# Kernel optimization log

Hardware: AMD Instinct MI355X
Metric: run time of the kernel (lower is better)

The kernel has to match this reference:

```python
import jax, jax.numpy as jnp
import numpy as np

N, E, IN, H, OUT = 100000, 1600000, 128, 128, 64


def setup_inputs() -> dict:
    key = jax.random.key(0)
    ks = jax.random.split(key, 7)
    x = jax.random.normal(ks[0], (N, IN), dtype=jnp.float32)
    edge_index = jax.random.randint(ks[1], (2, E), 0, N, dtype=jnp.int32)
    # Glorot-style scaled params (PyG SAGEConv: lin_l has bias, lin_r does not)
    s1 = 1.0 / np.sqrt(IN)
    s2 = 1.0 / np.sqrt(H)
    W1_l = jax.random.normal(ks[2], (H, IN), dtype=jnp.float32) * s1
    W1_r = jax.random.normal(ks[3], (H, IN), dtype=jnp.float32) * s1
    b1 = jnp.zeros((H,), dtype=jnp.float32)
    W2_l = jax.random.normal(ks[4], (OUT, H), dtype=jnp.float32) * s2
    W2_r = jax.random.normal(ks[5], (OUT, H), dtype=jnp.float32) * s2
    b2 = jnp.zeros((OUT,), dtype=jnp.float32)
    return {"x": x, "W1_l": W1_l, "W1_r": W1_r, "b1": b1,
            "W2_l": W2_l, "W2_r": W2_r, "b2": b2, "edge_index": edge_index}


def _sage_conv(x, edge_index, W_l, W_r, b):
    # mean-aggregate source-node features at target nodes, then linear + root term
    src, dst = edge_index[0], edge_index[1]
    n = x.shape[0]
    msgs = x[src]                                                   # [E, d]
    agg = jax.ops.segment_sum(msgs, dst, num_segments=n)            # [N, d]
    deg = jax.ops.segment_sum(jnp.ones((src.shape[0],), x.dtype), dst, num_segments=n)
    mean = agg / jnp.clip(deg, 1.0)[:, None]                        # zero-deg nodes stay 0
    return mean @ W_l.T + b + x @ W_r.T


def reference(x, W1_l, W1_r, b1, W2_l, W2_r, b2, edge_index):
    h = _sage_conv(x, edge_index, W1_l, W1_r, b1)
    h = jax.nn.relu(h)  # dropout p=0.0 -> identity
    out = _sage_conv(h, edge_index, W2_l, W2_r, b2)
    return out
```

## Files before the change

### kernel.cpp

```cpp
#include <hip/hip_runtime.h>


typedef unsigned int uint32;
typedef short bf16x4 __attribute__((ext_vector_type(4)));
typedef short bf16x8 __attribute__((ext_vector_type(8)));
typedef float f32x16 __attribute__((ext_vector_type(16)));
typedef float f32x2 __attribute__((ext_vector_type(2)));

#define PSTR 264

__device__ __forceinline__ uint32 pack_bf16_rne(float a, float b) {
    uint32 ua = __float_as_uint(a);
    uint32 ub = __float_as_uint(b);
    uint32 ra = (ua + 0x7fffu + ((ua >> 16) & 1u)) >> 16;
    uint32 rb = (ub + 0x7fffu + ((ub >> 16) & 1u)) >> 16;
    return ra | (rb << 16);
}
__device__ __forceinline__ float bf_lo(uint32 v) { return __uint_as_float(v << 16); }
__device__ __forceinline__ float bf_hi(uint32 v) { return __uint_as_float(v & 0xffff0000u); }

__device__ __forceinline__ short rne16(float v, float* back) {
    uint32 u = __float_as_uint(v);
    uint32 r = (u + 0x7fffu + ((u >> 16) & 1u)) >> 16;
    *back = __uint_as_float(r << 16);
    return (short)r;
}

__global__ void k_prep(const float* __restrict__ x, uint32* __restrict__ xb,
                       long n4,
                       const float* __restrict__ W1l, const float* __restrict__ W1r,
                       const float* __restrict__ W2l, const float* __restrict__ W2r,
                       short* __restrict__ W1pH, short* __restrict__ W1pL,
                       short* __restrict__ W2pH, short* __restrict__ W2pL) {
    long i = (long)blockIdx.x * blockDim.x + threadIdx.x;
    float back;
    if (i < n4) {
        float4 v = ((const float4*)x)[i];
        short h0 = rne16(v.x, &back);
        short h1 = rne16(v.y, &back);
        short h2 = rne16(v.z, &back);
        short h3 = rne16(v.w, &back);
        uint2 o;
        o.x = (uint32)(unsigned short)h0 | ((uint32)(unsigned short)h1 << 16);
        o.y = (uint32)(unsigned short)h2 | ((uint32)(unsigned short)h3 << 16);
        ((uint2*)xb)[i] = o;
        return;
    }
    int i2 = (int)(i - n4);
    if (i2 < 32768) {
        int j = i2 >> 8, k = i2 & 255;
        float v = (k < 128) ? W1l[j * 128 + k] : W1r[j * 128 + k - 128];
        float hb;
        short hs = rne16(v, &hb);
        short ls = rne16(v - hb, &back);
        int idx = (k >> 3) * 1024 + j * 8 + (k & 7);
        W1pH[idx] = hs;
        W1pL[idx] = ls;
    } else if (i2 < 32768 + 16384) {
        int i3 = i2 - 32768;
        int j = i3 >> 7, k = i3 & 127;
        float v = (j < 64) ? W2l[j * 128 + k] : W2r[(j - 64) * 128 + k];
        float hb;
        short hs = rne16(v, &hb);
        short ls = rne16(v - hb, &back);
        int idx = (k >> 3) * 1024 + j * 8 + (k & 7);
        W2pH[idx] = hs;
        W2pL[idx] = ls;
    }
}


__global__ void k_bcount(const int* __restrict__ ei, int E, int NB,
                         int* __restrict__ bucket_cnt) {
    __shared__ int hist[1024];
    int t = threadIdx.x;
    for (int i = t; i < NB; i += 256) hist[i] = 0;
    __syncthreads();
    int stride = gridDim.x * 256;
    for (int e = blockIdx.x * 256 + t; e < E; e += stride)
        atomicAdd(&hist[ei[E + e] >> 8], 1);
    __syncthreads();
    for (int i = t; i < NB; i += 256) {
        int c = hist[i];
        if (c) atomicAdd(&bucket_cnt[i], c);
    }
}

__global__ void k_bscan(const int* __restrict__ bucket_cnt, int NB, int E,
                        int* __restrict__ bucket_off, int* __restrict__ bucket_cur) {
    __shared__ int s[1024];
    int t = threadIdx.x;
    int v = (t < NB) ? bucket_cnt[t] : 0;
    s[t] = v;
    __syncthreads();
    for (int o = 1; o < 1024; o <<= 1) {
        int u = (t >= o) ? s[t - o] : 0;
        __syncthreads();
        s[t] += u;
        __syncthreads();
    }
    int ex = s[t] - v;
    if (t < NB) { bucket_off[t] = ex; bucket_cur[t] = ex; }
    if (t == NB - 1) bucket_off[NB] = ex + v;
}

__global__ void k_bscatter(const int* __restrict__ ei, int E, int NB,
                           int* __restrict__ bucket_cur, uint32* __restrict__ eb) {
    __shared__ int hist[1024];
    __shared__ int base[1024];
    int t = threadIdx.x;
    for (int i = t; i < NB; i += 256) hist[i] = 0;
    __syncthreads();
    int stride = gridDim.x * 256;
    for (int e = blockIdx.x * 256 + t; e < E; e += stride)
        atomicAdd(&hist[ei[E + e] >> 8], 1);
    __syncthreads();
    for (int i = t; i < NB; i += 256) {
        int c = hist[i];
        base[i] = c ? atomicAdd(&bucket_cur[i], c) : 0;
        hist[i] = 0;
    }
    __syncthreads();
    for (int e = blockIdx.x * 256 + t; e < E; e += stride) {
        int d = ei[E + e];
        int b = d >> 8;
        int r = atomicAdd(&hist[b], 1);
        eb[base[b] + r] = ((uint32)(d & 255) << 24) | (uint32)ei[e];
    }
}

__global__ void k_bfinal(const uint32* __restrict__ eb,
                         const int* __restrict__ bucket_off,
                         int* __restrict__ row_ptr, int* __restrict__ col,
                         int N, int E) {
    __shared__ int deg[256];
    __shared__ int sc[256];
    __shared__ int cur[256];
    int b = blockIdx.x;
    int t = threadIdx.x;
    int beg = bucket_off[b], end = bucket_off[b + 1];
    deg[t] = 0;
    __syncthreads();
    for (int e = beg + t; e < end; e += 256)
        atomicAdd(&deg[eb[e] >> 24], 1);
    __syncthreads();
    int v = deg[t];
    sc[t] = v;
    __syncthreads();
    for (int o = 1; o < 256; o <<= 1) {
        int u = (t >= o) ? sc[t - o] : 0;
        __syncthreads();
        sc[t] += u;
        __syncthreads();
    }
    int ex = sc[t] - v;
    int node = b * 256 + t;
    if (node < N) row_ptr[node] = beg + ex;
    if (b == gridDim.x - 1 && t == 0) row_ptr[N] = E;
    cur[t] = ex;
    __syncthreads();
    for (int e = beg + t; e < end; e += 256) {
        uint32 u = eb[e];
        int r = atomicAdd(&cur[u >> 24], 1);
        col[beg + r] = (int)(u & 0xFFFFFFu);
    }
}


__global__ __launch_bounds__(256, 4) void k_fused(
        const int* __restrict__ rp, const int* __restrict__ col,
        const uint32* __restrict__ xb,
        const short* __restrict__ W1pH, const short* __restrict__ W1pL,
        const short* __restrict__ W2pH, const short* __restrict__ W2pL,
        const float* __restrict__ b1, const float* __restrict__ b2,
        unsigned short* __restrict__ hl, float* __restrict__ hr, int N) {
    __shared__ short smH[16 * PSTR];
    __shared__ short smL[16 * PSTR];
    int t = threadIdx.x;
    int w = t >> 6, lane = t & 63;
    int g = lane >> 4, f = lane & 15;
    int node0 = blockIdx.x * 32;
    const uint4* xb4 = (const uint4*)xb;

    int base = node0 + 8 * w;
    int rpi = base + lane;
    if (rpi > N) rpi = N;
    int rpv = rp[rpi];

    for (int i = 0; i < 8; i++) {
        int lr = 8 * w + i;
        int beg = __builtin_amdgcn_readfirstlane(__shfl(rpv, i));
        int end = __builtin_amdgcn_readfirstlane(__shfl(rpv, i + 1));
        f32x2 sA[4];
#pragma unroll
        for (int j = 0; j < 4; j++) sA[j] = (f32x2){0.f, 0.f};

#define ACC_RAW(v)                                                      \
    { sA[0] += (f32x2){bf_lo(v.x), __uint_as_float(v.x)};               \
      sA[1] += (f32x2){bf_lo(v.y), __uint_as_float(v.y)};               \
      sA[2] += (f32x2){bf_lo(v.z), __uint_as_float(v.z)};               \
      sA[3] += (f32x2){bf_lo(v.w), __uint_as_float(v.w)}; }

        int e = beg;
        for (; e + 16 <= end; e += 16) {
            uint4 cv = *(const uint4*)(col + e + 4 * g);
            uint4 v0 = xb4[(size_t)cv.x * 16 + f];
            uint4 v1 = xb4[(size_t)cv.y * 16 + f];
            uint4 v2 = xb4[(size_t)cv.z * 16 + f];
            uint4 v3 = xb4[(size_t)cv.w * 16 + f];
            ACC_RAW(v0); ACC_RAW(v1); ACC_RAW(v2); ACC_RAW(v3);
        }
        for (; e + 8 <= end; e += 8) {
            uint2 cv = *(const uint2*)(col + e + 2 * g);
            uint4 v0 = xb4[(size_t)cv.x * 16 + f];
            uint4 v1 = xb4[(size_t)cv.y * 16 + f];
            ACC_RAW(v0); ACC_RAW(v1);
        }
        int rem = end - e;
        if (2 * g < rem) {
            uint4 v0 = xb4[(size_t)col[e + 2 * g] * 16 + f];
            ACC_RAW(v0);
        }
        if (2 * g + 1 < rem) {
            uint4 v0 = xb4[(size_t)col[e + 2 * g + 1] * 16 + f];
            ACC_RAW(v0);
        }
#undef ACC_RAW
#pragma unroll
        for (int p = 0; p < 4; p++) {
            sA[p].x += __shfl_xor(sA[p].x, 16);
            sA[p].y += __shfl_xor(sA[p].y, 16);
            sA[p].x += __shfl_xor(sA[p].x, 32);
            sA[p].y += __shfl_xor(sA[p].y, 32);
        }
        float inv = 1.0f / (float)max(end - beg, 1);
        float m0 = sA[g].x * inv, m1 = sA[g].y * inv;
        float b_;
        short h0 = rne16(m0, &b_);
        float bk0 = b_;
        short l0 = rne16(m0 - bk0, &b_);
        short h1 = rne16(m1, &b_);
        float bk1 = b_;
        short l1 = rne16(m1 - bk1, &b_);
        uint32 H = (uint32)(unsigned short)h0 | ((uint32)(unsigned short)h1 << 16);
        uint32 L = (uint32)(unsigned short)l0 | ((uint32)(unsigned short)l1 << 16);
        *(uint32*)&smH[f * PSTR + lr * 8 + 2 * g] = H;
        *(uint32*)&smL[f * PSTR + lr * 8 + 2 * g] = L;
    }
    __syncthreads();

    int m = lane & 31, hh = lane >> 5;
    int mynode = node0 + m;
    const short* xbs = (const short*)xb;
    f32x16 acc;
#pragma unroll
    for (int r = 0; r < 16; r++) acc[r] = 0.f;
#pragma unroll
    for (int kc = 0; kc < 8; kc++) {
        int c = 2 * kc + hh;
        bf16x8 bH = *(const bf16x8*)&smH[c * PSTR + m * 8];
        bf16x8 bL = *(const bf16x8*)&smL[c * PSTR + m * 8];
        bf16x8 xH = *(const bf16x8*)(xbs + (size_t)mynode * 128 + c * 8);
        bf16x8 aH1 = *(const bf16x8*)(W1pH + c * 1024 + (32 * w + m) * 8);
        bf16x8 aL1 = *(const bf16x8*)(W1pL + c * 1024 + (32 * w + m) * 8);
        bf16x8 aH2 = *(const bf16x8*)(W1pH + (16 + c) * 1024 + (32 * w + m) * 8);
        bf16x8 aL2 = *(const bf16x8*)(W1pL + (16 + c) * 1024 + (32 * w + m) * 8);
        acc = __builtin_amdgcn_mfma_f32_32x32x16_bf16(aH1, bH, acc, 0, 0, 0);
        acc = __builtin_amdgcn_mfma_f32_32x32x16_bf16(aL1, bH, acc, 0, 0, 0);
        acc = __builtin_amdgcn_mfma_f32_32x32x16_bf16(aH1, bL, acc, 0, 0, 0);
        acc = __builtin_amdgcn_mfma_f32_32x32x16_bf16(aH2, xH, acc, 0, 0, 0);
        acc = __builtin_amdgcn_mfma_f32_32x32x16_bf16(aL2, xH, acc, 0, 0, 0);
    }

    uint2 oh[4], ol[4];
#pragma unroll
    for (int rg = 0; rg < 4; rg++) {
        int j0 = 32 * w + 8 * rg + 4 * hh;
        float4 bv = *(const float4*)(b1 + j0);
        float bb[4] = {bv.x, bv.y, bv.z, bv.w};
        short hs[4], ls[4];
#pragma unroll
        for (int q = 0; q < 4; q++) {
            float v = fmaxf(acc[4 * rg + q] + bb[q], 0.f);
            float back;
            hs[q] = rne16(v, &back);
            ls[q] = rne16(v - back, &back);
        }
        oh[rg].x = (uint32)(unsigned short)hs[0] | ((uint32)(unsigned short)hs[1] << 16);
        oh[rg].y = (uint32)(unsigned short)hs[2] | ((uint32)(unsigned short)hs[3] << 16);
        ol[rg].x = (uint32)(unsigned short)ls[0] | ((uint32)(unsigned short)ls[1] << 16);
        ol[rg].y = (uint32)(unsigned short)ls[2] | ((uint32)(unsigned short)ls[3] << 16);
    }
    __syncthreads();
#pragma unroll
    for (int rg = 0; rg < 4; rg++) {
        int idx = (4 * w + rg) * PSTR + m * 8 + 4 * hh;
        *(uint2*)&smH[idx] = oh[rg];
        *(uint2*)&smL[idx] = ol[rg];
    }
    __syncthreads();

#pragma unroll
    for (int r = 0; r < 16; r++) acc[r] = 0.f;
#pragma unroll
    for (int kc = 0; kc < 8; kc++) {
        int c = 2 * kc + hh;
        bf16x8 bH = *(const bf16x8*)&smH[c * PSTR + m * 8];
        bf16x8 bL = *(const bf16x8*)&smL[c * PSTR + m * 8];
        bf16x8 aH = *(const bf16x8*)(W2pH + c * 1024 + (32 * w + m) * 8);
        bf16x8 aL = *(const bf16x8*)(W2pL + c * 1024 + (32 * w + m) * 8);
        acc = __builtin_amdgcn_mfma_f32_32x32x16_bf16(aH, bH, acc, 0, 0, 0);
        acc = __builtin_amdgcn_mfma_f32_32x32x16_bf16(aL, bH, acc, 0, 0, 0);
        acc = __builtin_amdgcn_mfma_f32_32x32x16_bf16(aH, bL, acc, 0, 0, 0);
    }
    if (mynode >= N) return;
    if (w < 2) {
#pragma unroll
        for (int rg = 0; rg < 4; rg++) {
            int j0 = 32 * w + 8 * rg + 4 * hh;
            uint2 o;
            o.x = pack_bf16_rne(acc[4 * rg + 0], acc[4 * rg + 1]);
            o.y = pack_bf16_rne(acc[4 * rg + 2], acc[4 * rg + 3]);
            *(uint2*)&hl[(size_t)mynode * 64 + j0] = o;
        }
    } else {
#pragma unroll
        for (int rg = 0; rg < 4; rg++) {
            int j0 = 32 * (w - 2) + 8 * rg + 4 * hh;
            float4 bv = *(const float4*)(b2 + j0);
            float4 o;
            o.x = acc[4 * rg + 0] + bv.x;
            o.y = acc[4 * rg + 1] + bv.y;
            o.z = acc[4 * rg + 2] + bv.z;
            o.w = acc[4 * rg + 3] + bv.w;
            *(float4*)&hr[(size_t)mynode * 64 + j0] = o;
        }
    }
}


__global__ void k_agg_out(const int* __restrict__ rp, const int* __restrict__ col,
                          const uint32* __restrict__ hl, const float* __restrict__ hr,
                          float* __restrict__ out, int N) {
    int node = blockIdx.x * 4 + (threadIdx.x >> 6);
    if (node >= N) return;
    node = __builtin_amdgcn_readfirstlane(node);
    int lane = threadIdx.x & 63;
    int g = lane >> 3;
    int f = lane & 7;
    int beg = rp[node], end = rp[node + 1];
    const uint4* hl4 = (const uint4*)hl;
    f32x2 sA[4];
#pragma unroll
    for (int j = 0; j < 4; j++) sA[j] = (f32x2){0.f, 0.f};

#define ACC_MSK(v)                                          \
    { sA[0] += (f32x2){bf_lo(v.x), bf_hi(v.x)};             \
      sA[1] += (f32x2){bf_lo(v.y), bf_hi(v.y)};             \
      sA[2] += (f32x2){bf_lo(v.z), bf_hi(v.z)};             \
      sA[3] += (f32x2){bf_lo(v.w), bf_hi(v.w)}; }

    int e = beg;
    for (; e + 16 <= end; e += 16) {
        uint2 cv = *(const uint2*)(col + e + 2 * g);
        uint4 v0 = hl4[(size_t)cv.x * 8 + f];
        uint4 v1 = hl4[(size_t)cv.y * 8 + f];
        ACC_MSK(v0); ACC_MSK(v1);
    }
    for (; e + 8 <= end; e += 8) {
        uint4 v0 = hl4[(size_t)col[e + g] * 8 + f];
        ACC_MSK(v0);
    }
    int rem = end - e;
    if (g < rem) {
        uint4 v0 = hl4[(size_t)col[e + g] * 8 + f];
        ACC_MSK(v0);
    }
#undef ACC_MSK
#pragma unroll
    for (int p = 0; p < 4; p++) {
        sA[p].x += __shfl_xor(sA[p].x, 8);
        sA[p].y += __shfl_xor(sA[p].y, 8);
        sA[p].x += __shfl_xor(sA[p].x, 16);
        sA[p].y += __shfl_xor(sA[p].y, 16);
        sA[p].x += __shfl_xor(sA[p].x, 32);
        sA[p].y += __shfl_xor(sA[p].y, 32);
    }
    if (g == 0) {
        float inv = 1.0f / (float)max(end - beg, 1);
        const float* hrp = hr + (size_t)node * 64 + f * 8;
        float4 h0 = *(const float4*)(hrp);
        float4 h1 = *(const float4*)(hrp + 4);
        float4 o0, o1;
        o0.x = sA[0].x * inv + h0.x;
        o0.y = sA[0].y * inv + h0.y;
        o0.z = sA[1].x * inv + h0.z;
        o0.w = sA[1].y * inv + h0.w;
        o1.x = sA[2].x * inv + h1.x;
        o1.y = sA[2].y * inv + h1.y;
        o1.z = sA[3].x * inv + h1.z;
        o1.w = sA[3].y * inv + h1.w;
        float* op = out + (size_t)node * 64 + f * 8;
        *(float4*)(op) = o0;
        *(float4*)(op + 4) = o1;
    }
}

extern "C" void kernel_launch(void* const* d_in, const int* in_sizes, int n_in,
                              void* d_out, int out_size, void* d_ws, size_t ws_size,
                              hipStream_t stream) {
    const float* x   = (const float*)d_in[0];
    const float* W1l = (const float*)d_in[1];
    const float* W1r = (const float*)d_in[2];
    const float* b1  = (const float*)d_in[3];
    const float* W2l = (const float*)d_in[4];
    const float* W2r = (const float*)d_in[5];
    const float* b2  = (const float*)d_in[6];
    const int*   ei  = (const int*)d_in[7];
    int N = in_sizes[0] / 128;
    int E = in_sizes[7] / 2;
    int NB = (N + 255) >> 8;
    int mb = (N + 31) / 32;
    int Np = ((N + 127) / 128) * 128;
    float* out = (float*)d_out;

    char* w = (char*)d_ws;
    size_t off = 0;
    auto alloc = [&](size_t bytes) -> char* {
        char* p = w + off;
        off += (bytes + 255) & ~(size_t)255;
        return p;
    };
    int*   row_ptr = (int*)alloc((size_t)(N + 1) * 4);
    int*   bcnt    = (int*)alloc((size_t)(NB + 1) * 4);
    int*   boff    = (int*)alloc((size_t)(NB + 1) * 4);
    int*   bcur    = (int*)alloc((size_t)(NB + 1) * 4);
    short* W1pH    = (short*)alloc(32768 * 2);
    short* W1pL    = (short*)alloc(32768 * 2);
    short* W2pH    = (short*)alloc(16384 * 2);
    short* W2pL    = (short*)alloc(16384 * 2);
    int*   col     = (int*)alloc((size_t)E * 4);
    uint32* xb     = (uint32*)alloc((size_t)Np * 64 * 4);
    float*  hr     = (float*)alloc((size_t)Np * 64 * 4);
    unsigned short* hl = (unsigned short*)alloc((size_t)N * 64 * 2);
    uint32* eb = (uint32*)hl;

    hipMemsetAsync(bcnt, 0, (size_t)NB * 4, stream);
    long n4 = (long)N * 32;
    long prep_items = n4 + 32768 + 16384;
    k_prep<<<(int)((prep_items + 255) / 256), 256, 0, stream>>>(
        x, xb, n4, W1l, W1r, W2l, W2r, W1pH, W1pL, W2pH, W2pL);
    k_bcount<<<256, 256, 0, stream>>>(ei, E, NB, bcnt);
    k_bscan<<<1, 1024, 0, stream>>>(bcnt, NB, E, boff, bcur);
    k_bscatter<<<128, 256, 0, stream>>>(ei, E, NB, bcur, eb);
    k_bfinal<<<NB, 256, 0, stream>>>(eb, boff, row_ptr, col, N, E);

    k_fused<<<mb, 256, 0, stream>>>(row_ptr, col, xb, W1pH, W1pL, W2pH, W2pL,
                                    b1, b2, hl, hr, N);
    int ab = (N + 3) / 4;
    k_agg_out<<<ab, 256, 0, stream>>>(row_ptr, col, (const uint32*)hl, hr, out, N);
}
```

Before: 316.8 us.

## Merge CSR-build launches and prefetch neighbor rows across nodes in aggregation

```diff
diff --git a/kernel.cpp b/kernel.cpp
--- a/kernel.cpp
+++ b/kernel.cpp
@@ -26,13 +26,31 @@
     return (short)r;
 }
 
-__global__ void k_prep(const float* __restrict__ x, uint32* __restrict__ xb,
-                       long n4,
-                       const float* __restrict__ W1l, const float* __restrict__ W1r,
-                       const float* __restrict__ W2l, const float* __restrict__ W2r,
-                       short* __restrict__ W1pH, short* __restrict__ W1pL,
-                       short* __restrict__ W2pH, short* __restrict__ W2pL) {
-    long i = (long)blockIdx.x * blockDim.x + threadIdx.x;
+__global__ void k_prepcount(const float* __restrict__ x, uint32* __restrict__ xb,
+                            long n4,
+                            const float* __restrict__ W1l, const float* __restrict__ W1r,
+                            const float* __restrict__ W2l, const float* __restrict__ W2r,
+                            short* __restrict__ W1pH, short* __restrict__ W1pL,
+                            short* __restrict__ W2pH, short* __restrict__ W2pL,
+                            const int* __restrict__ ei, int E, int NB,
+                            int* __restrict__ bucket_cnt, int prep_blocks) {
+    __shared__ int hist[512];
+    int t = threadIdx.x;
+    if ((int)blockIdx.x >= prep_blocks) {
+        int bb = (int)blockIdx.x - prep_blocks;
+        for (int i = t; i < NB; i += 256) hist[i] = 0;
+        __syncthreads();
+        int stride = 256 * 256;
+        for (int e = bb * 256 + t; e < E; e += stride)
+            atomicAdd(&hist[ei[E + e] >> 8], 1);
+        __syncthreads();
+        for (int i = t; i < NB; i += 256) {
+            int c = hist[i];
+            if (c) atomicAdd(&bucket_cnt[i], c);
+        }
+        return;
+    }
+    long i = (long)blockIdx.x * blockDim.x + t;
     float back;
     if (i < n4) {
         float4 v = ((const float4*)x)[i];
@@ -69,91 +87,87 @@
     }
 }
 
-
-__global__ void k_bcount(const int* __restrict__ ei, int E, int NB,
-                         int* __restrict__ bucket_cnt) {
-    __shared__ int hist[1024];
+__global__ void k_bscatter(const int* __restrict__ ei, int E, int NB,
+                           const int* __restrict__ bcnt, int* __restrict__ bcur,
+                           uint32* __restrict__ eb) {
+    __shared__ int sc[512];
+    __shared__ int hist[512];
+    __shared__ int basev[512];
     int t = threadIdx.x;
-    for (int i = t; i < NB; i += 256) hist[i] = 0;
-    __syncthreads();
+    int c0 = (t < NB) ? bcnt[t] : 0;
+    int c1 = (t + 256 < NB) ? bcnt[t + 256] : 0;
+    sc[t] = c0;
+    sc[t + 256] = c1;
+    hist[t] = 0;
+    hist[t + 256] = 0;
+    __syncthreads();
+    for (int o = 1; o < 512; o <<= 1) {
+        int a0 = (t >= o) ? sc[t - o] : 0;
+        int a1 = (t + 256 >= o) ? sc[t + 256 - o] : 0;
+        __syncthreads();
+        sc[t] += a0;
+        sc[t + 256] += a1;
+        __syncthreads();
+    }
     int stride = gridDim.x * 256;
     for (int e = blockIdx.x * 256 + t; e < E; e += stride)
         atomicAdd(&hist[ei[E + e] >> 8], 1);
     __syncthreads();
-    for (int i = t; i < NB; i += 256) {
-        int c = hist[i];
-        if (c) atomicAdd(&bucket_cnt[i], c);
-    }
-}
-
-__global__ void k_bscan(const int* __restrict__ bucket_cnt, int NB, int E,
-                        int* __restrict__ bucket_off, int* __restrict__ bucket_cur) {
-    __shared__ int s[1024];
-    int t = threadIdx.x;
-    int v = (t < NB) ? bucket_cnt[t] : 0;
-    s[t] = v;
-    __syncthreads();
-    for (int o = 1; o < 1024; o <<= 1) {
-        int u = (t >= o) ? s[t - o] : 0;
-        __syncthreads();
-        s[t] += u;
-        __syncthreads();
-    }
-    int ex = s[t] - v;
-    if (t < NB) { bucket_off[t] = ex; bucket_cur[t] = ex; }
-    if (t == NB - 1) bucket_off[NB] = ex + v;
-}
-
-__global__ void k_bscatter(const int* __restrict__ ei, int E, int NB,
-                           int* __restrict__ bucket_cur, uint32* __restrict__ eb) {
-    __shared__ int hist[1024];
-    __shared__ int base[1024];
-    int t = threadIdx.x;
-    for (int i = t; i < NB; i += 256) hist[i] = 0;
-    __syncthreads();
-    int stride = gridDim.x * 256;
-    for (int e = blockIdx.x * 256 + t; e < E; e += stride)
-        atomicAdd(&hist[ei[E + e] >> 8], 1);
-    __syncthreads();
-    for (int i = t; i < NB; i += 256) {
-        int c = hist[i];
-        base[i] = c ? atomicAdd(&bucket_cur[i], c) : 0;
-        hist[i] = 0;
+    {
+        int c = hist[t];
+        if (t < NB) basev[t] = (sc[t] - c0) + (c ? atomicAdd(&bcur[t], c) : 0);
+        hist[t] = 0;
+        int i1 = t + 256;
+        int c2 = hist[i1];
+        if (i1 < NB) basev[i1] = (sc[i1] - c1) + (c2 ? atomicAdd(&bcur[i1], c2) : 0);
+        hist[i1] = 0;
     }
     __syncthreads();
     for (int e = blockIdx.x * 256 + t; e < E; e += stride) {
         int d = ei[E + e];
         int b = d >> 8;
         int r = atomicAdd(&hist[b], 1);
-        eb[base[b] + r] = ((uint32)(d & 255) << 24) | (uint32)ei[e];
+        eb[basev[b] + r] = ((uint32)(d & 255) << 24) | (uint32)ei[e];
     }
 }
 
 __global__ void k_bfinal(const uint32* __restrict__ eb,
-                         const int* __restrict__ bucket_off,
+                         const int* __restrict__ bcnt,
                          int* __restrict__ row_ptr, int* __restrict__ col,
-                         int N, int E) {
+                         int N, int E, int NB) {
+    __shared__ int sc[512];
     __shared__ int deg[256];
-    __shared__ int sc[256];
+    __shared__ int scn[256];
     __shared__ int cur[256];
     int b = blockIdx.x;
     int t = threadIdx.x;
-    int beg = bucket_off[b], end = bucket_off[b + 1];
+    sc[t] = (t < NB) ? bcnt[t] : 0;
+    sc[t + 256] = (t + 256 < NB) ? bcnt[t + 256] : 0;
     deg[t] = 0;
     __syncthreads();
+    for (int o = 1; o < 512; o <<= 1) {
+        int a0 = (t >= o) ? sc[t - o] : 0;
+        int a1 = (t + 256 >= o) ? sc[t + 256 - o] : 0;
+        __syncthreads();
+        sc[t] += a0;
+        sc[t + 256] += a1;
+        __syncthreads();
+    }
+    int beg = (b > 0) ? sc[b - 1] : 0;
+    int end = sc[b];
     for (int e = beg + t; e < end; e += 256)
         atomicAdd(&deg[eb[e] >> 24], 1);
     __syncthreads();
     int v = deg[t];
-    sc[t] = v;
+    scn[t] = v;
     __syncthreads();
     for (int o = 1; o < 256; o <<= 1) {
-        int u = (t >= o) ? sc[t - o] : 0;
-        __syncthreads();
-        sc[t] += u;
-        __syncthreads();
-    }
-    int ex = sc[t] - v;
+        int u = (t >= o) ? scn[t - o] : 0;
+        __syncthreads();
+        scn[t] += u;
+        __syncthreads();
+    }
+    int ex = scn[t] - v;
     int node = b * 256 + t;
     if (node < N) row_ptr[node] = beg + ex;
     if (b == gridDim.x - 1 && t == 0) row_ptr[N] = E;
@@ -187,6 +201,26 @@
     if (rpi > N) rpi = N;
     int rpv = rp[rpi];
 
+    uint4 cvv[8];
+#pragma unroll
+    for (int i = 0; i < 8; i++) {
+        int bi = __shfl(rpv, i);
+        cvv[i] = *(const uint4*)(col + bi + 4 * g);
+    }
+    uint4 p0 = {}, p1 = {}, p2 = {}, p3 = {};
+    {
+        int b0 = __builtin_amdgcn_readfirstlane(__shfl(rpv, 0));
+        int e0 = __builtin_amdgcn_readfirstlane(__shfl(rpv, 1));
+        if (e0 - b0 >= 16) {
+            uint4 cvp = cvv[0];
+            p0 = xb4[(size_t)cvp.x * 16 + f];
+            p1 = xb4[(size_t)cvp.y * 16 + f];
+            p2 = xb4[(size_t)cvp.z * 16 + f];
+            p3 = xb4[(size_t)cvp.w * 16 + f];
+        }
+    }
+
+#pragma unroll
     for (int i = 0; i < 8; i++) {
         int lr = 8 * w + i;
         int beg = __builtin_amdgcn_readfirstlane(__shfl(rpv, i));
@@ -202,28 +236,49 @@
       sA[3] += (f32x2){bf_lo(v.w), __uint_as_float(v.w)}; }
 
         int e = beg;
-        for (; e + 16 <= end; e += 16) {
-            uint4 cv = *(const uint4*)(col + e + 4 * g);
-            uint4 v0 = xb4[(size_t)cv.x * 16 + f];
-            uint4 v1 = xb4[(size_t)cv.y * 16 + f];
-            uint4 v2 = xb4[(size_t)cv.z * 16 + f];
-            uint4 v3 = xb4[(size_t)cv.w * 16 + f];
+        bool has16 = (e + 16 <= end);
+        uint4 v0, v1, v2, v3;
+        if (has16) { v0 = p0; v1 = p1; v2 = p2; v3 = p3; }
+        if (i < 7) {
+            int nb = __builtin_amdgcn_readfirstlane(__shfl(rpv, i + 1));
+            int ne = __builtin_amdgcn_readfirstlane(__shfl(rpv, i + 2));
+            if (ne - nb >= 16) {
+                uint4 cvp = cvv[i + 1];
+                p0 = xb4[(size_t)cvp.x * 16 + f];
+                p1 = xb4[(size_t)cvp.y * 16 + f];
+                p2 = xb4[(size_t)cvp.z * 16 + f];
+                p3 = xb4[(size_t)cvp.w * 16 + f];
+            }
+        }
+        if (has16) {
+            uint4 cv = *(const uint4*)(col + e + 16 + 4 * g);
             ACC_RAW(v0); ACC_RAW(v1); ACC_RAW(v2); ACC_RAW(v3);
+            e += 16;
+            while (e + 16 <= end) {
+                uint4 w0 = xb4[(size_t)cv.x * 16 + f];
+                uint4 w1 = xb4[(size_t)cv.y * 16 + f];
+                uint4 w2 = xb4[(size_t)cv.z * 16 + f];
+                uint4 w3 = xb4[(size_t)cv.w * 16 + f];
+                uint4 cvn = *(const uint4*)(col + e + 16 + 4 * g);
+                ACC_RAW(w0); ACC_RAW(w1); ACC_RAW(w2); ACC_RAW(w3);
+                e += 16;
+                cv = cvn;
+            }
         }
         for (; e + 8 <= end; e += 8) {
-            uint2 cv = *(const uint2*)(col + e + 2 * g);
-            uint4 v0 = xb4[(size_t)cv.x * 16 + f];
-            uint4 v1 = xb4[(size_t)cv.y * 16 + f];
-            ACC_RAW(v0); ACC_RAW(v1);
+            uint2 cv2 = *(const uint2*)(col + e + 2 * g);
+            uint4 u0 = xb4[(size_t)cv2.x * 16 + f];
+            uint4 u1 = xb4[(size_t)cv2.y * 16 + f];
+            ACC_RAW(u0); ACC_RAW(u1);
         }
         int rem = end - e;
         if (2 * g < rem) {
-            uint4 v0 = xb4[(size_t)col[e + 2 * g] * 16 + f];
-            ACC_RAW(v0);
+            uint4 u0 = xb4[(size_t)col[e + 2 * g] * 16 + f];
+            ACC_RAW(u0);
         }
         if (2 * g + 1 < rem) {
-            uint4 v0 = xb4[(size_t)col[e + 2 * g + 1] * 16 + f];
-            ACC_RAW(v0);
+            uint4 u0 = xb4[(size_t)col[e + 2 * g + 1] * 16 + f];
+            ACC_RAW(u0);
         }
 #undef ACC_RAW
 #pragma unroll
@@ -360,12 +415,14 @@
       sA[2] += (f32x2){bf_lo(v.z), bf_hi(v.z)};             \
       sA[3] += (f32x2){bf_lo(v.w), bf_hi(v.w)}; }
 
+    uint2 cv = *(const uint2*)(col + beg + 2 * g);
     int e = beg;
     for (; e + 16 <= end; e += 16) {
-        uint2 cv = *(const uint2*)(col + e + 2 * g);
+        uint2 cvn = *(const uint2*)(col + e + 16 + 2 * g);
         uint4 v0 = hl4[(size_t)cv.x * 8 + f];
         uint4 v1 = hl4[(size_t)cv.y * 8 + f];
         ACC_MSK(v0); ACC_MSK(v1);
+        cv = cvn;
     }
     for (; e + 8 <= end; e += 8) {
         uint4 v0 = hl4[(size_t)col[e + g] * 8 + f];
@@ -432,9 +489,7 @@
         return p;
     };
     int*   row_ptr = (int*)alloc((size_t)(N + 1) * 4);
-    int*   bcnt    = (int*)alloc((size_t)(NB + 1) * 4);
-    int*   boff    = (int*)alloc((size_t)(NB + 1) * 4);
-    int*   bcur    = (int*)alloc((size_t)(NB + 1) * 4);
+    int*   bwork   = (int*)alloc((size_t)2 * (NB + 1) * 4);
     short* W1pH    = (short*)alloc(32768 * 2);
     short* W1pL    = (short*)alloc(32768 * 2);
     short* W2pH    = (short*)alloc(16384 * 2);
@@ -443,17 +498,19 @@
     uint32* xb     = (uint32*)alloc((size_t)Np * 64 * 4);
     float*  hr     = (float*)alloc((size_t)Np * 64 * 4);
     unsigned short* hl = (unsigned short*)alloc((size_t)N * 64 * 2);
+    int* bcnt = bwork;
+    int* bcur = bwork + (NB + 1);
     uint32* eb = (uint32*)hl;
 
-    hipMemsetAsync(bcnt, 0, (size_t)NB * 4, stream);
+    hipMemsetAsync(bwork, 0, (size_t)2 * (NB + 1) * 4, stream);
     long n4 = (long)N * 32;
     long prep_items = n4 + 32768 + 16384;
-    k_prep<<<(int)((prep_items + 255) / 256), 256, 0, stream>>>(
-        x, xb, n4, W1l, W1r, W2l, W2r, W1pH, W1pL, W2pH, W2pL);
-    k_bcount<<<256, 256, 0, stream>>>(ei, E, NB, bcnt);
-    k_bscan<<<1, 1024, 0, stream>>>(bcnt, NB, E, boff, bcur);
-    k_bscatter<<<128, 256, 0, stream>>>(ei, E, NB, bcur, eb);
-    k_bfinal<<<NB, 256, 0, stream>>>(eb, boff, row_ptr, col, N, E);
+    int prep_blocks = (int)((prep_items + 255) / 256);
+    k_prepcount<<<prep_blocks + 256, 256, 0, stream>>>(
+        x, xb, n4, W1l, W1r, W2l, W2r, W1pH, W1pL, W2pH, W2pL,
+        ei, E, NB, bcnt, prep_blocks);
+    k_bscatter<<<128, 256, 0, stream>>>(ei, E, NB, bcnt, bcur, eb);
+    k_bfinal<<<NB, 256, 0, stream>>>(eb, bcnt, row_ptr, col, N, E, NB);
 
     k_fused<<<mb, 256, 0, stream>>>(row_ptr, col, xb, W1pH, W1pL, W2pH, W2pL,
                                     b1, b2, hl, hr, N);
```

Result: slower. 340.4 us (+7.4%).

## Gather neighbor rows with one lane per feature element, dropping cross-lane reductions

Applied to the files above, without the earlier changes.

```diff
diff --git a/kernel.cpp b/kernel.cpp
--- a/kernel.cpp
+++ b/kernel.cpp
@@ -2,7 +2,6 @@
 
 
 typedef unsigned int uint32;
-typedef short bf16x4 __attribute__((ext_vector_type(4)));
 typedef short bf16x8 __attribute__((ext_vector_type(8)));
 typedef float f32x16 __attribute__((ext_vector_type(16)));
 typedef float f32x2 __attribute__((ext_vector_type(2)));
@@ -17,7 +16,6 @@
     return ra | (rb << 16);
 }
 __device__ __forceinline__ float bf_lo(uint32 v) { return __uint_as_float(v << 16); }
-__device__ __forceinline__ float bf_hi(uint32 v) { return __uint_as_float(v & 0xffff0000u); }
 
 __device__ __forceinline__ short rne16(float v, float* back) {
     uint32 u = __float_as_uint(v);
@@ -178,63 +176,49 @@
     __shared__ short smL[16 * PSTR];
     int t = threadIdx.x;
     int w = t >> 6, lane = t & 63;
-    int g = lane >> 4, f = lane & 15;
     int node0 = blockIdx.x * 32;
-    const uint4* xb4 = (const uint4*)xb;
 
     int base = node0 + 8 * w;
     int rpi = base + lane;
     if (rpi > N) rpi = N;
     int rpv = rp[rpi];
 
+#define ACC1(a) { s += (f32x2){bf_lo(a), __uint_as_float(a)}; }
+
     for (int i = 0; i < 8; i++) {
         int lr = 8 * w + i;
         int beg = __builtin_amdgcn_readfirstlane(__shfl(rpv, i));
         int end = __builtin_amdgcn_readfirstlane(__shfl(rpv, i + 1));
-        f32x2 sA[4];
-#pragma unroll
-        for (int j = 0; j < 4; j++) sA[j] = (f32x2){0.f, 0.f};
-
-#define ACC_RAW(v)                                                      \
-    { sA[0] += (f32x2){bf_lo(v.x), __uint_as_float(v.x)};               \
-      sA[1] += (f32x2){bf_lo(v.y), __uint_as_float(v.y)};               \
-      sA[2] += (f32x2){bf_lo(v.z), __uint_as_float(v.z)};               \
-      sA[3] += (f32x2){bf_lo(v.w), __uint_as_float(v.w)}; }
-
+        f32x2 s = (f32x2){0.f, 0.f};
         int e = beg;
-        for (; e + 16 <= end; e += 16) {
-            uint4 cv = *(const uint4*)(col + e + 4 * g);
-            uint4 v0 = xb4[(size_t)cv.x * 16 + f];
-            uint4 v1 = xb4[(size_t)cv.y * 16 + f];
-            uint4 v2 = xb4[(size_t)cv.z * 16 + f];
-            uint4 v3 = xb4[(size_t)cv.w * 16 + f];
-            ACC_RAW(v0); ACC_RAW(v1); ACC_RAW(v2); ACC_RAW(v3);
-        }
         for (; e + 8 <= end; e += 8) {
-            uint2 cv = *(const uint2*)(col + e + 2 * g);
-            uint4 v0 = xb4[(size_t)cv.x * 16 + f];
-            uint4 v1 = xb4[(size_t)cv.y * 16 + f];
-            ACC_RAW(v0); ACC_RAW(v1);
-        }
-        int rem = end - e;
-        if (2 * g < rem) {
-            uint4 v0 = xb4[(size_t)col[e + 2 * g] * 16 + f];
-            ACC_RAW(v0);
-        }
-        if (2 * g + 1 < rem) {
-            uint4 v0 = xb4[(size_t)col[e + 2 * g + 1] * 16 + f];
-            ACC_RAW(v0);
-        }
-#undef ACC_RAW
-#pragma unroll
-        for (int p = 0; p < 4; p++) {
-            sA[p].x += __shfl_xor(sA[p].x, 16);
-            sA[p].y += __shfl_xor(sA[p].y, 16);
-            sA[p].x += __shfl_xor(sA[p].x, 32);
-            sA[p].y += __shfl_xor(sA[p].y, 32);
+            int c0 = col[e + 0], c1 = col[e + 1], c2 = col[e + 2], c3 = col[e + 3];
+            int c4 = col[e + 4], c5 = col[e + 5], c6 = col[e + 6], c7 = col[e + 7];
+            uint32 a0 = xb[(size_t)c0 * 64 + lane];
+            uint32 a1 = xb[(size_t)c1 * 64 + lane];
+            uint32 a2 = xb[(size_t)c2 * 64 + lane];
+            uint32 a3 = xb[(size_t)c3 * 64 + lane];
+            uint32 a4 = xb[(size_t)c4 * 64 + lane];
+            uint32 a5 = xb[(size_t)c5 * 64 + lane];
+            uint32 a6 = xb[(size_t)c6 * 64 + lane];
+            uint32 a7 = xb[(size_t)c7 * 64 + lane];
+            ACC1(a0); ACC1(a1); ACC1(a2); ACC1(a3);
+            ACC1(a4); ACC1(a5); ACC1(a6); ACC1(a7);
+        }
+        for (; e + 4 <= end; e += 4) {
+            int c0 = col[e + 0], c1 = col[e + 1], c2 = col[e + 2], c3 = col[e + 3];
+            uint32 a0 = xb[(size_t)c0 * 64 + lane];
+            uint32 a1 = xb[(size_t)c1 * 64 + lane];
+            uint32 a2 = xb[(size_t)c2 * 64 + lane];
+            uint32 a3 = xb[(size_t)c3 * 64 + lane];
+            ACC1(a0); ACC1(a1); ACC1(a2); ACC1(a3);
+        }
+        for (; e < end; e++) {
+            uint32 a0 = xb[(size_t)col[e] * 64 + lane];
+            ACC1(a0);
         }
         float inv = 1.0f / (float)max(end - beg, 1);
-        float m0 = sA[g].x * inv, m1 = sA[g].y * inv;
+        float m0 = s.x * inv, m1 = s.y * inv;
         float b_;
         short h0 = rne16(m0, &b_);
         float bk0 = b_;
@@ -244,9 +228,11 @@
         short l1 = rne16(m1 - bk1, &b_);
         uint32 H = (uint32)(unsigned short)h0 | ((uint32)(unsigned short)h1 << 16);
         uint32 L = (uint32)(unsigned short)l0 | ((uint32)(unsigned short)l1 << 16);
-        *(uint32*)&smH[f * PSTR + lr * 8 + 2 * g] = H;
-        *(uint32*)&smL[f * PSTR + lr * 8 + 2 * g] = L;
-    }
+        int idx = (lane >> 2) * PSTR + lr * 8 + 2 * (lane & 3);
+        *(uint32*)&smH[idx] = H;
+        *(uint32*)&smL[idx] = L;
+    }
+#undef ACC1
     __syncthreads();
 
     int m = lane & 31, hh = lane >> 5;
@@ -340,70 +326,48 @@
 
 
 __global__ void k_agg_out(const int* __restrict__ rp, const int* __restrict__ col,
-                          const uint32* __restrict__ hl, const float* __restrict__ hr,
+                          const unsigned short* __restrict__ hl,
+                          const float* __restrict__ hr,
                           float* __restrict__ out, int N) {
     int node = blockIdx.x * 4 + (threadIdx.x >> 6);
     if (node >= N) return;
     node = __builtin_amdgcn_readfirstlane(node);
     int lane = threadIdx.x & 63;
-    int g = lane >> 3;
-    int f = lane & 7;
     int beg = rp[node], end = rp[node + 1];
-    const uint4* hl4 = (const uint4*)hl;
-    f32x2 sA[4];
-#pragma unroll
-    for (int j = 0; j < 4; j++) sA[j] = (f32x2){0.f, 0.f};
-
-#define ACC_MSK(v)                                          \
-    { sA[0] += (f32x2){bf_lo(v.x), bf_hi(v.x)};             \
-      sA[1] += (f32x2){bf_lo(v.y), bf_hi(v.y)};             \
-      sA[2] += (f32x2){bf_lo(v.z), bf_hi(v.z)};             \
-      sA[3] += (f32x2){bf_lo(v.w), bf_hi(v.w)}; }
+    float s = 0.f;
+
+#define ACCU(a) { s += __uint_as_float((uint32)(a) << 16); }
 
     int e = beg;
-    for (; e + 16 <= end; e += 16) {
-        uint2 cv = *(const uint2*)(col + e + 2 * g);
-        uint4 v0 = hl4[(size_t)cv.x * 8 + f];
-        uint4 v1 = hl4[(size_t)cv.y * 8 + f];
-        ACC_MSK(v0); ACC_MSK(v1);
-    }
     for (; e + 8 <= end; e += 8) {
-        uint4 v0 = hl4[(size_t)col[e + g] * 8 + f];
-        ACC_MSK(v0);
-    }
-    int rem = end - e;
-    if (g < rem) {
-        uint4 v0 = hl4[(size_t)col[e + g] * 8 + f];
-        ACC_MSK(v0);
-    }
-#undef ACC_MSK
-#pragma unroll
-    for (int p = 0; p < 4; p++) {
-        sA[p].x += __shfl_xor(sA[p].x, 8);
-        sA[p].y += __shfl_xor(sA[p].y, 8);
-        sA[p].x += __shfl_xor(sA[p].x, 16);
-        sA[p].y += __shfl_xor(sA[p].y, 16);
-        sA[p].x += __shfl_xor(sA[p].x, 32);
-        sA[p].y += __shfl_xor(sA[p].y, 32);
-    }
-    if (g == 0) {
-        float inv = 1.0f / (float)max(end - beg, 1);
-        const float* hrp = hr + (size_t)node * 64 + f * 8;
-        float4 h0 = *(const float4*)(hrp);
-        float4 h1 = *(const float4*)(hrp + 4);
-        float4 o0, o1;
-        o0.x = sA[0].x * inv + h0.x;
-        o0.y = sA[0].y * inv + h0.y;
-        o0.z = sA[1].x * inv + h0.z;
-        o0.w = sA[1].y * inv + h0.w;
-        o1.x = sA[2].x * inv + h1.x;
-        o1.y = sA[2].y * inv + h1.y;
-        o1.z = sA[3].x * inv + h1.z;
-        o1.w = sA[3].y * inv + h1.w;
-        float* op = out + (size_t)node * 64 + f * 8;
-        *(float4*)(op) = o0;
-        *(float4*)(op + 4) = o1;
-    }
+        int c0 = col[e + 0], c1 = col[e + 1], c2 = col[e + 2], c3 = col[e + 3];
+        int c4 = col[e + 4], c5 = col[e + 5], c6 = col[e + 6], c7 = col[e + 7];
+        unsigned short a0 = hl[(size_t)c0 * 64 + lane];
+        unsigned short a1 = hl[(size_t)c1 * 64 + lane];
+        unsigned short a2 = hl[(size_t)c2 * 64 + lane];
+        unsigned short a3 = hl[(size_t)c3 * 64 + lane];
+        unsigned short a4 = hl[(size_t)c4 * 64 + lane];
+        unsigned short a5 = hl[(size_t)c5 * 64 + lane];
+        unsigned short a6 = hl[(size_t)c6 * 64 + lane];
+        unsigned short a7 = hl[(size_t)c7 * 64 + lane];
+        ACCU(a0); ACCU(a1); ACCU(a2); ACCU(a3);
+        ACCU(a4); ACCU(a5); ACCU(a6); ACCU(a7);
+    }
+    for (; e + 4 <= end; e += 4) {
+        int c0 = col[e + 0], c1 = col[e + 1], c2 = col[e + 2], c3 = col[e + 3];
+        unsigned short a0 = hl[(size_t)c0 * 64 + lane];
+        unsigned short a1 = hl[(size_t)c1 * 64 + lane];
+        unsigned short a2 = hl[(size_t)c2 * 64 + lane];
+        unsigned short a3 = hl[(size_t)c3 * 64 + lane];
+        ACCU(a0); ACCU(a1); ACCU(a2); ACCU(a3);
+    }
+    for (; e < end; e++) {
+        unsigned short a0 = hl[(size_t)col[e] * 64 + lane];
+        ACCU(a0);
+    }
+#undef ACCU
+    float inv = 1.0f / (float)max(end - beg, 1);
+    out[(size_t)node * 64 + lane] = s * inv + hr[(size_t)node * 64 + lane];
 }
 
 extern "C" void kernel_launch(void* const* d_in, const int* in_sizes, int n_in,
@@ -458,5 +422,5 @@
     k_fused<<<mb, 256, 0, stream>>>(row_ptr, col, xb, W1pH, W1pL, W2pH, W2pL,
                                     b1, b2, hl, hr, N);
     int ab = (N + 3) / 4;
-    k_agg_out<<<ab, 256, 0, stream>>>(row_ptr, col, (const uint32*)hl, hr, out, N);
-}
+    k_agg_out<<<ab, 256, 0, stream>>>(row_ptr, col, hl, hr, out, N);
+}
```

After: 318.7 us. No clear change (+0.6%).
